# Optimization experiments

Measured on AMD Instinct MI355X. Metric: run time of the kernel, lower is better.

The kernel has to match this reference:

```python
import jax, jax.numpy as jnp
import numpy as np

N = 100000
IN_C = 128
HID_C = 128
OUT_C = 128
E = 3200000


def setup_inputs() -> dict:
    key = jax.random.key(0)
    ks = jax.random.split(key, 8)
    x = jax.random.normal(ks[0], (N, IN_C), dtype=jnp.float32)
    edge_index = jax.random.randint(ks[1], (2, E), 0, N, dtype=jnp.int64)
    edge_weight = jnp.ones((E,), dtype=jnp.float32)
    s = 1.0 / np.sqrt(HID_C)
    W_conv = jax.random.uniform(ks[2], (HID_C, IN_C), jnp.float32, -s, s)
    b_conv = jnp.zeros((HID_C,), dtype=jnp.float32)
    W_fc = jax.random.uniform(ks[3], (HID_C, HID_C), jnp.float32, -s, s)
    b_fc = jax.random.uniform(ks[4], (HID_C,), jnp.float32, -s, s)
    W_fc2 = jax.random.uniform(ks[5], (OUT_C, HID_C), jnp.float32, -s, s)
    b_fc2 = jax.random.uniform(ks[6], (OUT_C,), jnp.float32, -s, s)
    return {"x": x, "edge_index": edge_index, "edge_weight": edge_weight,
            "W_conv": W_conv, "b_conv": b_conv, "W_fc": W_fc, "b_fc": b_fc,
            "W_fc2": W_fc2, "b_fc2": b_fc2}


def _gcn_conv(x, edge_index, edge_weight, W_conv, b_conv):
    n = x.shape[0]
    # add self-loops with weight 1 (PyG GCNConv default)
    loop = jnp.arange(n, dtype=edge_index.dtype)
    src = jnp.concatenate([edge_index[0], loop])
    dst = jnp.concatenate([edge_index[1], loop])
    ew = jnp.concatenate([edge_weight, jnp.ones((n,), dtype=edge_weight.dtype)])
    # symmetric normalization: deg^-1/2[src] * w * deg^-1/2[dst]
    deg = jax.ops.segment_sum(ew, dst, num_segments=n)
    dinv = jnp.where(deg > 0, jax.lax.rsqrt(jnp.where(deg > 0, deg, 1.0)), 0.0)
    norm = dinv[src] * ew * dinv[dst]  # [E+N]
    h = x @ W_conv.T                   # [N, hid], bias-free linear first
    msg = h[src] * norm[:, None]       # gather + scale
    agg = jax.ops.segment_sum(msg, dst, num_segments=n)  # scatter-add
    return agg + b_conv


def reference(x, edge_index, edge_weight, W_conv, b_conv, W_fc, b_fc, W_fc2, b_fc2):
    h = _gcn_conv(x, edge_index, edge_weight, W_conv, b_conv)
    h = jax.nn.relu(h)
    h = jax.nn.relu(h @ W_fc.T + b_fc)
    return h @ W_fc2.T + b_fc2
```

## Files before the change

### kernel.cpp

```cpp
#include <hip/hip_runtime.h>

typedef short bf16x8 __attribute__((ext_vector_type(8)));
typedef short bf16x4 __attribute__((ext_vector_type(4)));
typedef float f32x4 __attribute__((ext_vector_type(4)));
typedef float f32x2 __attribute__((ext_vector_type(2)));

#define PS 32
#define PMAX 4096
#define CAPP 1312
#define NB 256

__device__ __forceinline__ unsigned short f2bf(float f) {
    unsigned int u = __float_as_uint(f);
    u = (u + 0x7FFFu + ((u >> 16) & 1u)) >> 16;
    return (unsigned short)u;
}

__global__ __launch_bounds__(1024) void scat_k(const int* __restrict__ ei,
                                               const float* __restrict__ ew,
                                               int* __restrict__ partCnt,
                                               int2* __restrict__ regions,
                                               const float* __restrict__ Wc,
                                               const float* __restrict__ Wf,
                                               const float* __restrict__ W2,
                                               unsigned short* __restrict__ wcb,
                                               unsigned short* __restrict__ wfb,
                                               unsigned short* __restrict__ w2b,
                                               int E, int P, int EPB) {
    __shared__ int cntl[PMAX];
    __shared__ int basel[PMAX];
    const int b = blockIdx.x, tid = threadIdx.x;

    if (b < 12) {
        int t = (b << 10) | tid;
        int a = t >> 12, idx = t & 4095;
        const float4* s4 = (const float4*)(a == 0 ? Wc : (a == 1 ? Wf : W2));
        unsigned short* dw = (a == 0 ? wcb : (a == 1 ? wfb : w2b));
        float4 v = s4[idx];
        ushort4 o;
        o.x = f2bf(v.x); o.y = f2bf(v.y); o.z = f2bf(v.z); o.w = f2bf(v.w);
        *(ushort4*)(dw + idx * 4) = o;
    }

    for (int i = tid; i < P; i += 1024) cntl[i] = 0;
    __syncthreads();
    const int s = b * EPB, e = min(E, s + EPB);
    for (int i = s + tid; i < e; i += 1024)
        atomicAdd(&cntl[ei[E + i] >> 5], 1);
    __syncthreads();
    for (int p = tid; p < P; p += 1024) {
        int c = cntl[p];
        basel[p] = p * CAPP + (c ? atomicAdd(&partCnt[p], c) : 0);
        cntl[p] = 0;
    }
    __syncthreads();
    for (int i = s + tid; i < e; i += 1024) {
        int src = ei[i];
        int dst = ei[E + i];
        float w = ew[i];
        int p = dst >> 5, dl = dst & 31;
        int lidx = atomicAdd(&cntl[p], 1);
        int pos = basel[p] + lidx;
        if (pos < (p + 1) * CAPP)
            regions[pos] = make_int2(src | (dl << 24), __float_as_int(w));
    }
}

__global__ __launch_bounds__(256) void dgemm1_k(const float* __restrict__ x,
                                                const unsigned short* __restrict__ Wcb,
                                                const int* __restrict__ partCnt,
                                                const int2* __restrict__ regions,
                                                float* __restrict__ dinv,
                                                int* __restrict__ nodeOff,
                                                unsigned short* __restrict__ h,
                                                int M, int P) {
    __shared__ __align__(16) unsigned short Wl[128 * 136];
    __shared__ float degl[64];
    __shared__ int cl[64];
    __shared__ float dl64[64];
    const int tid = threadIdx.x;
    if (tid < 64) { degl[tid] = 0.f; cl[tid] = 0; }

#pragma unroll
    for (int i = 0; i < 8; ++i) {
        int c = i * 256 + tid;
        int r = c >> 4, col = (c & 15) * 8;
        *(bf16x8*)&Wl[r * 136 + col] = *(const bf16x8*)(Wcb + c * 8);
    }
    __syncthreads();

#pragma unroll
    for (int q = 0; q < 2; ++q) {
        int p = blockIdx.x * 2 + q;
        if (p < P) {
            const int cnt = min(partCnt[p], CAPP);
            const int2* reg = regions + (size_t)p * CAPP;
            for (int i = tid; i < cnt; i += 256) {
                int2 r = reg[i];
                int dl = q * 32 + ((r.x >> 24) & 31);
                atomicAdd(&cl[dl], 1);
                atomicAdd(&degl[dl], __int_as_float(r.y));
            }
        }
    }
    __syncthreads();
    if (tid < 64) {
        int cn = cl[tid];
        int v = cn;
#pragma unroll
        for (int off = 1; off < 32; off <<= 1) {
            int u = __shfl_up(v, off, 32);
            if ((tid & 31) >= off) v += u;
        }
        int node = blockIdx.x * 64 + tid;
        float d = rsqrtf(1.0f + degl[tid]);
        if (node < M) { nodeOff[node] = v - cn; dinv[node] = d; }
        dl64[tid] = d;
    }
    __syncthreads();

    const int wave = tid >> 6, lane = tid & 63;
    const int m = lane & 15, quad = lane >> 4;
    const int rowBase = blockIdx.x * 64 + wave * 16;
    int arow = rowBase + m;
    int arowc = arow < M ? arow : (M - 1);

    bf16x8 afrag[4];
    const float* pa = x + (size_t)arowc * 128 + quad * 8;
#pragma unroll
    for (int kc = 0; kc < 4; ++kc) {
        float4 v0 = *(const float4*)(pa + kc * 32);
        float4 v1 = *(const float4*)(pa + kc * 32 + 4);
        bf16x8 f;
        f[0] = (short)f2bf(v0.x); f[1] = (short)f2bf(v0.y);
        f[2] = (short)f2bf(v0.z); f[3] = (short)f2bf(v0.w);
        f[4] = (short)f2bf(v1.x); f[5] = (short)f2bf(v1.y);
        f[6] = (short)f2bf(v1.z); f[7] = (short)f2bf(v1.w);
        afrag[kc] = f;
    }

    float dv[4];
#pragma unroll
    for (int r = 0; r < 4; ++r)
        dv[r] = dl64[wave * 16 + quad * 4 + r];

#pragma unroll
    for (int nt = 0; nt < 8; ++nt) {
        f32x4 acc = {0.f, 0.f, 0.f, 0.f};
        const unsigned short* wb = &Wl[(nt * 16 + m) * 136 + quad * 8];
#pragma unroll
        for (int kc = 0; kc < 4; ++kc) {
            bf16x8 bfrag = *(const bf16x8*)(wb + kc * 32);
            acc = __builtin_amdgcn_mfma_f32_16x16x32_bf16(afrag[kc], bfrag, acc, 0, 0, 0);
        }
        const int col = nt * 16 + m;
#pragma unroll
        for (int r = 0; r < 4; ++r) {
            int row = rowBase + quad * 4 + r;
            if (row < M)
                h[((size_t)(col >> 6) * M + row) * 64 + (col & 63)] = f2bf(acc[r] * dv[r]);
        }
    }
}

__global__ __launch_bounds__(256) void aggF_k(const int* __restrict__ partCnt,
                                              const int* __restrict__ nodeOff,
                                              const int2* __restrict__ regions,
                                              const unsigned short* __restrict__ h,
                                              const float* __restrict__ dinv,
                                              const float* __restrict__ bconv,
                                              unsigned short* __restrict__ h2, int N) {
    __shared__ __align__(16) int2 stag[CAPP];
    __shared__ int cstart[PS + 1];
    __shared__ int wcur[PS];
    const int p = blockIdx.x, tid = threadIdx.x;
    const int cnt = min(partCnt[p], CAPP);
    const int2* reg = regions + (size_t)p * CAPP;

    if (tid < PS) {
        int node = p * PS + tid;
        int o = (node < N) ? nodeOff[node] : cnt;
        cstart[tid] = o;
        wcur[tid] = o;
    } else if (tid == PS) {
        cstart[PS] = cnt;
    }
    __syncthreads();
    for (int i = tid; i < cnt; i += 256) {
        int2 r = reg[i];
        int pos = atomicAdd(&wcur[(r.x >> 24) & 31], 1);
        stag[pos] = make_int2((r.x & 0xFFFFFF) << 7, r.y);
    }
    __syncthreads();

    const int wave = tid >> 6, lane = tid & 63;
    const int g = lane >> 4;
    const int c4 = (lane & 15) * 4;
    const int c4b = c4 * 2;

#define ACC2(q, w) {                                                        \
        unsigned ux = (unsigned)(q).x, uy = (unsigned)(q).y;                \
        f32x2 ww; ww[0] = (w); ww[1] = (w);                                 \
        f32x2 v01, v23;                                                     \
        v01[0] = __uint_as_float(ux << 16);                                 \
        v01[1] = __uint_as_float(ux & 0xFFFF0000u);                         \
        v23[0] = __uint_as_float(uy << 16);                                 \
        v23[1] = __uint_as_float(uy & 0xFFFF0000u);                         \
        a01 = v01 * ww + a01; a23 = v23 * ww + a23; }

#pragma unroll
    for (int hh = 0; hh < 2; ++hh) {
        const char* hb = (const char*)h + ((size_t)hh * (size_t)N << 7);
        for (int nl = wave; nl < PS; nl += 4) {
            int n = p * PS + nl;
            if (n >= N) continue;
            const int s = cstart[nl], e = cstart[nl + 1];
            f32x2 a01 = {0.f, 0.f}, a23 = {0.f, 0.f};
            int j = s;
            const int e32 = s + ((e - s) & ~31);
            for (; j < e32; j += 32) {
                int2 r0 = stag[j + g];
                int2 r1 = stag[j + 4 + g];
                int2 r2 = stag[j + 8 + g];
                int2 r3 = stag[j + 12 + g];
                int2 r4 = stag[j + 16 + g];
                int2 r5 = stag[j + 20 + g];
                int2 r6 = stag[j + 24 + g];
                int2 r7 = stag[j + 28 + g];
                int2 q0 = *(const int2*)(hb + ((unsigned)r0.x + c4b));
                int2 q1 = *(const int2*)(hb + ((unsigned)r1.x + c4b));
                int2 q2 = *(const int2*)(hb + ((unsigned)r2.x + c4b));
                int2 q3 = *(const int2*)(hb + ((unsigned)r3.x + c4b));
                int2 q4 = *(const int2*)(hb + ((unsigned)r4.x + c4b));
                int2 q5 = *(const int2*)(hb + ((unsigned)r5.x + c4b));
                int2 q6 = *(const int2*)(hb + ((unsigned)r6.x + c4b));
                int2 q7 = *(const int2*)(hb + ((unsigned)r7.x + c4b));
                ACC2(q0, __int_as_float(r0.y));
                ACC2(q1, __int_as_float(r1.y));
                ACC2(q2, __int_as_float(r2.y));
                ACC2(q3, __int_as_float(r3.y));
                ACC2(q4, __int_as_float(r4.y));
                ACC2(q5, __int_as_float(r5.y));
                ACC2(q6, __int_as_float(r6.y));
                ACC2(q7, __int_as_float(r7.y));
            }
            const int e16 = s + ((e - s) & ~15);
            for (; j < e16; j += 16) {
                int2 r0 = stag[j + g];
                int2 r1 = stag[j + 4 + g];
                int2 r2 = stag[j + 8 + g];
                int2 r3 = stag[j + 12 + g];
                int2 q0 = *(const int2*)(hb + ((unsigned)r0.x + c4b));
                int2 q1 = *(const int2*)(hb + ((unsigned)r1.x + c4b));
                int2 q2 = *(const int2*)(hb + ((unsigned)r2.x + c4b));
                int2 q3 = *(const int2*)(hb + ((unsigned)r3.x + c4b));
                ACC2(q0, __int_as_float(r0.y));
                ACC2(q1, __int_as_float(r1.y));
                ACC2(q2, __int_as_float(r2.y));
                ACC2(q3, __int_as_float(r3.y));
            }
            for (; j < e; j += 8) {
                int j0 = j + g, j1 = j + 4 + g;
                int2 r0 = stag[j0 < e ? j0 : s];
                int2 r1 = stag[j1 < e ? j1 : s];
                float w0 = (j0 < e) ? __int_as_float(r0.y) : 0.f;
                float w1 = (j1 < e) ? __int_as_float(r1.y) : 0.f;
                int2 q0 = *(const int2*)(hb + ((unsigned)r0.x + c4b));
                int2 q1 = *(const int2*)(hb + ((unsigned)r1.x + c4b));
                ACC2(q0, w0);
                ACC2(q1, w1);
            }
            float acc[4] = {a01[0], a01[1], a23[0], a23[1]};
#pragma unroll
            for (int k = 0; k < 4; ++k) {
                float v = acc[k];
                v += __shfl_xor(v, 16, 64);
                v += __shfl_xor(v, 32, 64);
                acc[k] = v;
            }
            if (g == 0) {
                float di = dinv[n];
                int2 qs = *(const int2*)(hb + (((size_t)(unsigned)n << 7) + c4b));
                float4 b = *(const float4*)(bconv + hh * 64 + c4);
                unsigned ux = (unsigned)qs.x, uy = (unsigned)qs.y;
                bf16x4 o;
                o[0] = (short)f2bf(fmaxf(di * (acc[0] + __uint_as_float(ux << 16)) + b.x, 0.f));
                o[1] = (short)f2bf(fmaxf(di * (acc[1] + __uint_as_float(ux & 0xFFFF0000u)) + b.y, 0.f));
                o[2] = (short)f2bf(fmaxf(di * (acc[2] + __uint_as_float(uy << 16)) + b.z, 0.f));
                o[3] = (short)f2bf(fmaxf(di * (acc[3] + __uint_as_float(uy & 0xFFFF0000u)) + b.w, 0.f));
                *(bf16x4*)(h2 + (size_t)n * 128 + hh * 64 + c4) = o;
            }
        }
    }
#undef ACC2
}

__global__ __launch_bounds__(256) void gemm23_k(const unsigned short* __restrict__ h2,
                                                const unsigned short* __restrict__ Wfb,
                                                const float* __restrict__ bfc,
                                                const unsigned short* __restrict__ W2b,
                                                const float* __restrict__ b2,
                                                float* __restrict__ out, int M) {
    __shared__ __align__(16) unsigned short Wl[128 * 136];
    __shared__ __align__(16) unsigned short Tl[64 * 136];
    const int tid = threadIdx.x;

#pragma unroll
    for (int i = 0; i < 8; ++i) {
        int c = i * 256 + tid;
        int r = c >> 4, col = (c & 15) * 8;
        *(bf16x8*)&Wl[r * 136 + col] = *(const bf16x8*)(Wfb + c * 8);
    }
    __syncthreads();

    const int wave = tid >> 6, lane = tid & 63;
    const int m = lane & 15, quad = lane >> 4;
    const int rowBase = blockIdx.x * 64 + wave * 16;
    int arow = rowBase + m;
    int arowc = arow < M ? arow : (M - 1);

    bf16x8 afrag[4];
    {
        const unsigned short* pa = h2 + (size_t)arowc * 128 + quad * 8;
#pragma unroll
        for (int kc = 0; kc < 4; ++kc)
            afrag[kc] = *(const bf16x8*)(pa + kc * 32);
    }

#pragma unroll
    for (int nt = 0; nt < 8; ++nt) {
        f32x4 acc = {0.f, 0.f, 0.f, 0.f};
        const unsigned short* wb = &Wl[(nt * 16 + m) * 136 + quad * 8];
#pragma unroll
        for (int kc = 0; kc < 4; ++kc) {
            bf16x8 bfrag = *(const bf16x8*)(wb + kc * 32);
            acc = __builtin_amdgcn_mfma_f32_16x16x32_bf16(afrag[kc], bfrag, acc, 0, 0, 0);
        }
        const int col = nt * 16 + m;
        float bv = bfc[col];
#pragma unroll
        for (int r = 0; r < 4; ++r) {
            int rowl = wave * 16 + quad * 4 + r;
            Tl[rowl * 136 + col] = f2bf(fmaxf(acc[r] + bv, 0.f));
        }
    }
    __syncthreads();

#pragma unroll
    for (int i = 0; i < 8; ++i) {
        int c = i * 256 + tid;
        int r = c >> 4, col = (c & 15) * 8;
        *(bf16x8*)&Wl[r * 136 + col] = *(const bf16x8*)(W2b + c * 8);
    }
    __syncthreads();

    bf16x8 afrag2[4];
    {
        const unsigned short* pa = &Tl[(wave * 16 + m) * 136 + quad * 8];
#pragma unroll
        for (int kc = 0; kc < 4; ++kc)
            afrag2[kc] = *(const bf16x8*)(pa + kc * 32);
    }
#pragma unroll
    for (int nt = 0; nt < 8; ++nt) {
        f32x4 acc = {0.f, 0.f, 0.f, 0.f};
        const unsigned short* wb = &Wl[(nt * 16 + m) * 136 + quad * 8];
#pragma unroll
        for (int kc = 0; kc < 4; ++kc) {
            bf16x8 bfrag = *(const bf16x8*)(wb + kc * 32);
            acc = __builtin_amdgcn_mfma_f32_16x16x32_bf16(afrag2[kc], bfrag, acc, 0, 0, 0);
        }
        const int col = nt * 16 + m;
        float bv = b2[col];
#pragma unroll
        for (int r = 0; r < 4; ++r) {
            int row = rowBase + quad * 4 + r;
            if (row < M)
                out[(size_t)row * 128 + col] = acc[r] + bv;
        }
    }
}

extern "C" void kernel_launch(void* const* d_in, const int* in_sizes, int n_in,
                              void* d_out, int out_size, void* d_ws, size_t ws_size,
                              hipStream_t stream) {
    const float* x  = (const float*)d_in[0];
    const int* ei   = (const int*)d_in[1];
    const float* ew = (const float*)d_in[2];
    const float* Wc = (const float*)d_in[3];
    const float* bc = (const float*)d_in[4];
    const float* Wf = (const float*)d_in[5];
    const float* bf = (const float*)d_in[6];
    const float* W2 = (const float*)d_in[7];
    const float* b2 = (const float*)d_in[8];
    float* out = (float*)d_out;

    const int N = in_sizes[0] / 128;
    const int E = in_sizes[2];
    const int P = (N + PS - 1) / PS;

    auto align256 = [](size_t v) { return (v + 255) & ~(size_t)255; };
    char* ws = (char*)d_ws;
    size_t off = 0;
    float* dinv  = (float*)(ws + off); off += align256((size_t)N * 4);
    int* nodeOff = (int*)(ws + off);   off += align256((size_t)N * 4);
    int* partCnt = (int*)(ws + off);   off += align256((size_t)P * 4);
    unsigned short* wcb = (unsigned short*)(ws + off); off += align256(16384 * 2);
    unsigned short* wfb = (unsigned short*)(ws + off); off += align256(16384 * 2);
    unsigned short* w2b = (unsigned short*)(ws + off); off += align256(16384 * 2);
    unsigned short* h  = (unsigned short*)(ws + off); off += (size_t)N * 256;
    unsigned short* h2 = (unsigned short*)(ws + off);

    int2* regions = (int2*)out;

    const int EPB = (E + NB - 1) / NB;

    hipMemsetAsync(partCnt, 0, (size_t)P * 4, stream);
    scat_k<<<NB, 1024, 0, stream>>>(ei, ew, partCnt, regions, Wc, Wf, W2, wcb, wfb, w2b, E, P, EPB);
    dgemm1_k<<<(N + 63) / 64, 256, 0, stream>>>(x, wcb, partCnt, regions, dinv, nodeOff, h, N, P);
    aggF_k<<<P, 256, 0, stream>>>(partCnt, nodeOff, regions, h, dinv, bc, h2, N);
    gemm23_k<<<(N + 63) / 64, 256, 0, stream>>>(h2, wfb, bf, w2b, b2, out, N);
}
```

Measured before the change: 364.1 us.

## Split edge partitioning into two-pass radix scatter via coarse buckets

Replaces the single-pass edge scatter into 3125 fine partitions with a two-pass scheme. Edges are first binned into about 196 coarse buckets of 512 nodes each, staged in the h buffer, and then redistributed per bucket into 32-node partitions. The aim is fewer per-block global atomics and better write locality, since each block's writes now land in a few large contiguous runs. The cost is an extra kernel launch and a full extra read and write of the edge records. It also relies on node ids fitting in 17 bits and on bucket sizes staying under CAPB.

```diff
diff --git a/kernel.cpp b/kernel.cpp
--- a/kernel.cpp
+++ b/kernel.cpp
@@ -6,9 +6,9 @@
 typedef float f32x2 __attribute__((ext_vector_type(2)));
 
 #define PS 32
-#define PMAX 4096
 #define CAPP 1312
 #define NB 256
+#define CAPB 17536
 
 __device__ __forceinline__ unsigned short f2bf(float f) {
     unsigned int u = __float_as_uint(f);
@@ -16,19 +16,19 @@
     return (unsigned short)u;
 }
 
-__global__ __launch_bounds__(1024) void scat_k(const int* __restrict__ ei,
-                                               const float* __restrict__ ew,
-                                               int* __restrict__ partCnt,
-                                               int2* __restrict__ regions,
-                                               const float* __restrict__ Wc,
-                                               const float* __restrict__ Wf,
-                                               const float* __restrict__ W2,
-                                               unsigned short* __restrict__ wcb,
-                                               unsigned short* __restrict__ wfb,
-                                               unsigned short* __restrict__ w2b,
-                                               int E, int P, int EPB) {
-    __shared__ int cntl[PMAX];
-    __shared__ int basel[PMAX];
+__global__ __launch_bounds__(1024) void scatA_k(const int* __restrict__ ei,
+                                                const float* __restrict__ ew,
+                                                int* __restrict__ bucketCnt,
+                                                int2* __restrict__ bstage,
+                                                const float* __restrict__ Wc,
+                                                const float* __restrict__ Wf,
+                                                const float* __restrict__ W2,
+                                                unsigned short* __restrict__ wcb,
+                                                unsigned short* __restrict__ wfb,
+                                                unsigned short* __restrict__ w2b,
+                                                int E, int NBK, int EPB) {
+    __shared__ int cntl[256];
+    __shared__ int basel[256];
     const int b = blockIdx.x, tid = threadIdx.x;
 
     if (b < 12) {
@@ -42,27 +42,63 @@
         *(ushort4*)(dw + idx * 4) = o;
     }
 
-    for (int i = tid; i < P; i += 1024) cntl[i] = 0;
+    if (tid < 256) cntl[tid] = 0;
     __syncthreads();
     const int s = b * EPB, e = min(E, s + EPB);
     for (int i = s + tid; i < e; i += 1024)
-        atomicAdd(&cntl[ei[E + i] >> 5], 1);
-    __syncthreads();
-    for (int p = tid; p < P; p += 1024) {
-        int c = cntl[p];
-        basel[p] = p * CAPP + (c ? atomicAdd(&partCnt[p], c) : 0);
-        cntl[p] = 0;
+        atomicAdd(&cntl[ei[E + i] >> 9], 1);
+    __syncthreads();
+    if (tid < NBK) {
+        int c = cntl[tid];
+        basel[tid] = tid * CAPB + (c ? atomicAdd(&bucketCnt[tid], c) : 0);
+        cntl[tid] = 0;
     }
     __syncthreads();
     for (int i = s + tid; i < e; i += 1024) {
         int src = ei[i];
         int dst = ei[E + i];
         float w = ew[i];
-        int p = dst >> 5, dl = dst & 31;
-        int lidx = atomicAdd(&cntl[p], 1);
-        int pos = basel[p] + lidx;
-        if (pos < (p + 1) * CAPP)
-            regions[pos] = make_int2(src | (dl << 24), __float_as_int(w));
+        int bk = dst >> 9;
+        int lidx = atomicAdd(&cntl[bk], 1);
+        int pos = basel[bk] + lidx;
+        if (pos < (bk + 1) * CAPB)
+            bstage[pos] = make_int2(src | ((dst & 31) << 17) | (((dst >> 5) & 15) << 22),
+                                    __float_as_int(w));
+    }
+}
+
+__global__ __launch_bounds__(1024) void scatB_k(const int* __restrict__ bucketCnt,
+                                                const int2* __restrict__ bstage,
+                                                int* __restrict__ partCnt,
+                                                int2* __restrict__ regions,
+                                                int P) {
+    __shared__ int cl[16];
+    __shared__ int cur[16];
+    const int bk = blockIdx.x, tid = threadIdx.x;
+    const int cnt = min(bucketCnt[bk], CAPB);
+    const int2* bs = bstage + (size_t)bk * CAPB;
+
+    if (tid < 16) cl[tid] = 0;
+    __syncthreads();
+    for (int i = tid; i < cnt; i += 1024)
+        atomicAdd(&cl[((unsigned)bs[i].x >> 22) & 15], 1);
+    __syncthreads();
+    if (tid < 16) {
+        int p = bk * 16 + tid;
+        if (p < P) partCnt[p] = cl[tid];
+        cur[tid] = 0;
+    }
+    __syncthreads();
+    for (int i = tid; i < cnt; i += 1024) {
+        int2 r = bs[i];
+        unsigned x = (unsigned)r.x;
+        int pl = (x >> 22) & 15;
+        int pos = atomicAdd(&cur[pl], 1);
+        if (pos < CAPP) {
+            int p = bk * 16 + pl;
+            regions[(size_t)p * CAPP + pos] =
+                make_int2((int)(x & 0x1FFFFu) | (int)(((x >> 17) & 31u) << 24), r.y);
+        }
     }
 }
 
@@ -398,6 +434,7 @@
     const int N = in_sizes[0] / 128;
     const int E = in_sizes[2];
     const int P = (N + PS - 1) / PS;
+    const int NBK = (N + 511) >> 9;
 
     auto align256 = [](size_t v) { return (v + 255) & ~(size_t)255; };
     char* ws = (char*)d_ws;
@@ -405,18 +442,22 @@
     float* dinv  = (float*)(ws + off); off += align256((size_t)N * 4);
     int* nodeOff = (int*)(ws + off);   off += align256((size_t)N * 4);
     int* partCnt = (int*)(ws + off);   off += align256((size_t)P * 4);
+    int* bucketCnt = (int*)(ws + off); off += align256((size_t)NBK * 4);
     unsigned short* wcb = (unsigned short*)(ws + off); off += align256(16384 * 2);
     unsigned short* wfb = (unsigned short*)(ws + off); off += align256(16384 * 2);
     unsigned short* w2b = (unsigned short*)(ws + off); off += align256(16384 * 2);
     unsigned short* h  = (unsigned short*)(ws + off); off += (size_t)N * 256;
     unsigned short* h2 = (unsigned short*)(ws + off);
 
+    int2* bstage = (int2*)h;
+
     int2* regions = (int2*)out;
 
     const int EPB = (E + NB - 1) / NB;
 
-    hipMemsetAsync(partCnt, 0, (size_t)P * 4, stream);
-    scat_k<<<NB, 1024, 0, stream>>>(ei, ew, partCnt, regions, Wc, Wf, W2, wcb, wfb, w2b, E, P, EPB);
+    hipMemsetAsync(bucketCnt, 0, (size_t)NBK * 4, stream);
+    scatA_k<<<NB, 1024, 0, stream>>>(ei, ew, bucketCnt, bstage, Wc, Wf, W2, wcb, wfb, w2b, E, NBK, EPB);
+    scatB_k<<<NBK, 1024, 0, stream>>>(bucketCnt, bstage, partCnt, regions, P);
     dgemm1_k<<<(N + 63) / 64, 256, 0, stream>>>(x, wcb, partCnt, regions, dinv, nodeOff, h, N, P);
     aggF_k<<<P, 256, 0, stream>>>(partCnt, nodeOff, regions, h, dinv, bc, h2, N);
     gemm23_k<<<(N + 63) / 64, 256, 0, stream>>>(h2, wfb, bf, w2b, b2, out, N);
```

After: 337.5 us. 1.08x faster.
